# Kernel tuning notes

Hardware: AMD Instinct MI355X
Metric: run time of the kernel (lower is better)

The kernel has to match this reference:

```python
import jax, jax.numpy as jnp
import numpy as np

D_MODEL = 1024
NUM_HEADS = 16
HEAD_DIM = 64
INNER = NUM_HEADS * HEAD_DIM


def setup_inputs() -> dict:
    key = jax.random.key(0)
    k_x, k_q, k_k, k_v, k_o = jax.random.split(key, 5)
    B, T = 4, 2048
    s = 1.0 / np.sqrt(D_MODEL)
    return {
        "x": jax.random.normal(k_x, (B, T, D_MODEL), dtype=jnp.float32),
        "W_q": jax.random.uniform(k_q, (D_MODEL, INNER), dtype=jnp.float32, minval=-s, maxval=s),
        "W_k": jax.random.uniform(k_k, (D_MODEL, INNER), dtype=jnp.float32, minval=-s, maxval=s),
        "W_v": jax.random.uniform(k_v, (D_MODEL, INNER), dtype=jnp.float32, minval=-s, maxval=s),
        "W_o": jax.random.uniform(k_o, (INNER, D_MODEL), dtype=jnp.float32, minval=-s, maxval=s),
    }


def reference(x, W_q, W_k, W_v, W_o):
    B, T, _ = x.shape
    scale = HEAD_DIM ** -0.5
    # project and split heads: [B, H, T, Dh]
    q = (x @ W_q).reshape(B, T, NUM_HEADS, HEAD_DIM).transpose(0, 2, 1, 3)
    k = (x @ W_k).reshape(B, T, NUM_HEADS, HEAD_DIM).transpose(0, 2, 1, 3)
    v = (x @ W_v).reshape(B, T, NUM_HEADS, HEAD_DIM).transpose(0, 2, 1, 3)
    scores = jnp.einsum("bhqd,bhkd->bhqk", q, k) * scale  # [B,H,T,T]
    causal = jnp.tril(jnp.ones((T, T), dtype=bool))
    scores = jnp.where(causal, scores, -jnp.inf)
    probs = jax.nn.softmax(scores, axis=-1)
    ctx = jnp.einsum("bhqk,bhkd->bhqd", probs, v)
    ctx = ctx.transpose(0, 2, 1, 3).reshape(B, T, INNER)
    return ctx @ W_o
```

## Files before the change

kernel.cpp:

```cpp
#include <hip/hip_runtime.h>


typedef short  short8  __attribute__((ext_vector_type(8)));
typedef short  short4v __attribute__((ext_vector_type(4)));
typedef float  floatx4 __attribute__((ext_vector_type(4)));
typedef unsigned uint2v __attribute__((ext_vector_type(2)));

#define T_SZ 2048
#define DM   1024

#define QSCALE 0.18033688011112042f

__device__ __forceinline__ short f2bf(float f) {
  unsigned u = __float_as_uint(f);
  u += 0x7fffu + ((u >> 16) & 1u);
  return (short)(u >> 16);
}

#if defined(__has_builtin) && __has_builtin(__builtin_amdgcn_cvt_pk_bf16_f32)
typedef __bf16 bf16x2_t __attribute__((ext_vector_type(2)));
__device__ __forceinline__ unsigned pack_bf(float lo, float hi) {
  return __builtin_bit_cast(unsigned, __builtin_amdgcn_cvt_pk_bf16_f32(lo, hi));
}
#else
__device__ __forceinline__ unsigned pack_bf(float lo, float hi) {
  return __builtin_amdgcn_perm(__float_as_uint(hi) + 0x8000u,
                               __float_as_uint(lo) + 0x8000u, 0x07060302u);
}
#endif

#if defined(__has_builtin) && __has_builtin(__builtin_amdgcn_exp2f)
__device__ __forceinline__ float fexp2(float x) { return __builtin_amdgcn_exp2f(x); }
#else
__device__ __forceinline__ float fexp2(float x) { return exp2f(x); }
#endif

__device__ __forceinline__ void gll16(const void* g, void* l) {
  __builtin_amdgcn_global_load_lds((const __attribute__((address_space(1))) void*)g,
                                   (__attribute__((address_space(3))) void*)l, 16, 0, 0);
}

__global__ void cvt_kernel(const float* __restrict__ s0, const float* __restrict__ s1,
                           const float* __restrict__ s2, const float* __restrict__ s3,
                           short* __restrict__ dst,
                           const float* __restrict__ x, short* __restrict__ xb) {
  const int tx = threadIdx.x, ty = threadIdx.y;
  if (blockIdx.z == 4) {
    const int tid = ty * 32 + tx;
    const int blk = blockIdx.y * 32 + blockIdx.x;
    int i = (blk * 256 + tid) * 4;
#pragma unroll
    for (int j = 0; j < 8; ++j) {
      const float4 v = *(const float4*)(x + i);
      short4v o;
      o.x = f2bf(v.x); o.y = f2bf(v.y); o.z = f2bf(v.z); o.w = f2bf(v.w);
      *(short4v*)(xb + i) = o;
      i += 1048576;
    }
    return;
  }
  const float* srcs[4] = {s0, s1, s2, s3};
  const float* src = srcs[blockIdx.z];
  short* d = dst + (size_t)blockIdx.z * 1048576;
  __shared__ float tile[32][33];
  const int n_base = blockIdx.x * 32, k_base = blockIdx.y * 32;
#pragma unroll
  for (int j = 0; j < 4; ++j)
    tile[ty + j * 8][tx] = src[(size_t)(k_base + ty + j * 8) * 1024 + n_base + tx];
  __syncthreads();
#pragma unroll
  for (int j = 0; j < 4; ++j)
    d[(size_t)(n_base + ty + j * 8) * 1024 + k_base + tx] = f2bf(tile[tx][ty + j * 8]);
}

template <int MODE>
__global__ void gemm_bt(const short* __restrict__ A, const short* __restrict__ Bt,
                        short* __restrict__ obf, short* __restrict__ vt,
                        float* __restrict__ of, int K) {
  __shared__ short As[128 * 32];
  __shared__ short Bs[128 * 32];
  const int tid  = threadIdx.x;
  const int w    = tid >> 6, lane = tid & 63;
  const int quad = lane >> 4, l15 = lane & 15;
  const int wr   = w >> 1, wc = w & 1;
  const int lid  = (int)blockIdx.y * 64 + (int)blockIdx.x;
  const int m0   = (((lid & 7) + 8 * ((lid >> 3) & 7))) * 128;
  const int n0   = (lid >> 6) * 128;
  const int arow = tid >> 2, apart = tid & 3;

  floatx4 acc[4][4] = {};

  for (int kk = 0; kk < K; kk += 32) {
    gll16(A  + (size_t)(m0 + arow) * K      + kk + apart * 8, &As[tid * 8]);
    gll16(A  + (size_t)(m0 + 64 + arow) * K + kk + apart * 8, &As[(256 + tid) * 8]);
    gll16(Bt + (size_t)(n0 + arow) * K      + kk + apart * 8, &Bs[tid * 8]);
    gll16(Bt + (size_t)(n0 + 64 + arow) * K + kk + apart * 8, &Bs[(256 + tid) * 8]);
    __syncthreads();
    short8 af[4], bfr[4];
#pragma unroll
    for (int i = 0; i < 4; ++i)
      af[i] = *(const short8*)&As[(wr * 64 + i * 16 + l15) * 32 + quad * 8];
#pragma unroll
    for (int j = 0; j < 4; ++j)
      bfr[j] = *(const short8*)&Bs[(wc * 64 + j * 16 + l15) * 32 + quad * 8];
#pragma unroll
    for (int i = 0; i < 4; ++i)
#pragma unroll
      for (int j = 0; j < 4; ++j)
        acc[i][j] = __builtin_amdgcn_mfma_f32_16x16x32_bf16(af[i], bfr[j], acc[i][j], 0, 0, 0);
    __syncthreads();
  }

  if (MODE == 0) {
    const int wsel = n0 >> 10;
    const int ncol0 = (n0 & 1023) + wc * 64;
    if (wsel < 2) {
      const float scale = (wsel == 0) ? QSCALE : 1.0f;
      short* outw = obf + (size_t)wsel * (64u * 2048u * 64u);
#pragma unroll
      for (int i = 0; i < 4; ++i) {
        const int row0 = m0 + wr * 64 + i * 16 + quad * 4;
#pragma unroll
        for (int j = 0; j < 4; ++j) {
          const int col = ncol0 + j * 16 + l15;
          const int h = col >> 6, d = col & 63;
#pragma unroll
          for (int r = 0; r < 4; ++r) {
            const int rg = row0 + r;
            const int b = rg >> 11, t = rg & 2047;
            outw[(((size_t)(b * 16 + h) * 2048 + t) << 6) + d] = f2bf(acc[i][j][r] * scale);
          }
        }
      }
    } else {
#pragma unroll
      for (int i = 0; i < 4; ++i) {
        const int row0 = m0 + wr * 64 + i * 16 + quad * 4;
        const int b = row0 >> 11, t = row0 & 2047;
#pragma unroll
        for (int j = 0; j < 4; ++j) {
          const int col = ncol0 + j * 16 + l15;
          const int h = col >> 6, d = col & 63;
          short4v pv;
#pragma unroll
          for (int r = 0; r < 4; ++r) pv[r] = f2bf(acc[i][j][r]);
          *(short4v*)(vt + (((size_t)(b * 16 + h) * 64 + d) << 11) + t) = pv;
        }
      }
    }
  } else {
#pragma unroll
    for (int i = 0; i < 4; ++i) {
      const int row0 = m0 + wr * 64 + i * 16 + quad * 4;
#pragma unroll
      for (int j = 0; j < 4; ++j) {
        const int col = n0 + wc * 64 + j * 16 + l15;
#pragma unroll
        for (int r = 0; r < 4; ++r)
          of[(size_t)(row0 + r) * 1024 + col] = acc[i][j][r];
      }
    }
  }
}

__global__ __launch_bounds__(512, 4) void attn_kernel(
    const short* __restrict__ Qg, const short* __restrict__ Kg,
    const short* __restrict__ Vt, short* __restrict__ ctx) {
  __shared__ short Ks[128 * 72];
  __shared__ short Vs[80 * 136];
  __shared__ short Ps[8 * 32 * 40];

  const int tid  = threadIdx.x;
  const int w    = tid >> 6, lane = tid & 63;
  const int quad = lane >> 4, l15 = lane & 15;
  const int bh = (int)blockIdx.x + 8 * ((int)blockIdx.y & 7);
  const int g  = (int)blockIdx.y >> 3;
  const int qb = (g < 4) ? (7 - g) : (g - 4);
  const int b  = bh >> 4, h = bh & 15;

  const size_t base = (size_t)bh * (T_SZ * 64);
  const short* Qb  = Qg + base;
  const short* Kb  = Kg + base;
  const short* Vtb = Vt + base;
  short* Pw = &Ps[w * 1280];

  const int skr = tid >> 2, skp = (tid & 3) * 16;
  const int svr = tid >> 3, svp = (tid & 7) * 16;

  if (tid < 256) {
    const int rr = 64 + (tid >> 4), cb = (tid & 15) * 8;
    const short vv = (tid < 16) ? (short)0x3F80 : (short)0;
    short8 fill;
#pragma unroll
    for (int j = 0; j < 8; ++j) fill[j] = vv;
    *(short8*)&Vs[rr * 136 + cb] = fill;
  }

  const int rowA = qb * 256 + w * 32;
  const int rowB = rowA + 16;
  const int ktmax = 2 * qb + 2;

  const short8 qA0 = *(const short8*)(Qb + (size_t)(rowA + l15) * 64 + quad * 8);
  const short8 qA1 = *(const short8*)(Qb + (size_t)(rowA + l15) * 64 + 32 + quad * 8);
  const short8 qB0 = *(const short8*)(Qb + (size_t)(rowB + l15) * 64 + quad * 8);
  const short8 qB1 = *(const short8*)(Qb + (size_t)(rowB + l15) * 64 + 32 + quad * 8);

  floatx4 OA[4] = {}, OB[4] = {};
  floatx4 O5A = {}, O5B = {};

  short8 kR[2], vR[2];
  kR[0] = *(const short8*)(Kb + (size_t)skr * 64 + skp);
  kR[1] = *(const short8*)(Kb + (size_t)skr * 64 + skp + 8);
  vR[0] = *(const short8*)(Vtb + (size_t)svr * 2048 + svp);
  vR[1] = *(const short8*)(Vtb + (size_t)svr * 2048 + svp + 8);

  for (int kt = 0; kt < ktmax; ++kt) {
    const int k0 = kt << 7;
    __syncthreads();
    *(short8*)&Ks[skr * 72 + skp]     = kR[0];
    *(short8*)&Ks[skr * 72 + skp + 8] = kR[1];
    *(short8*)&Vs[svr * 136 + svp]     = vR[0];
    *(short8*)&Vs[svr * 136 + svp + 8] = vR[1];
    if (kt + 1 < ktmax) {
      const int kn = (kt + 1) << 7;
      kR[0] = *(const short8*)(Kb + (size_t)(kn + skr) * 64 + skp);
      kR[1] = *(const short8*)(Kb + (size_t)(kn + skr) * 64 + skp + 8);
      vR[0] = *(const short8*)(Vtb + (size_t)svr * 2048 + kn + svp);
      vR[1] = *(const short8*)(Vtb + (size_t)svr * 2048 + kn + svp + 8);
    }
    __syncthreads();

    const int dkA = rowA - k0;
    if (dkA < 0) continue;
    const int dkB = dkA + 16;
    const int limA = dkA + l15, limB = limA + 16;
    const int naA = min(8, (dkA >> 4) + 1), nchA = (naA + 1) >> 1;
    const int naB = min(8, (dkB >> 4) + 1), nchB = (naB + 1) >> 1;

#pragma unroll
    for (int c = 0; c < 4; ++c) {
      if (c < nchB) {
#pragma unroll
        for (int mm = 0; mm < 2; ++mm) {
          const int mt = 2 * c + mm;
          const int pa = l15 * 40 + mm * 16 + quad * 4;
          const int pb = (16 + l15) * 40 + mm * 16 + quad * 4;
          const bool aB = (mt * 16 < dkB + 16);
          const bool aA = (mt * 16 < dkA + 16);
          if (aB) {
            const short8 kf0 = *(const short8*)&Ks[(mt * 16 + l15) * 72 + quad * 8];
            const short8 kf1 = *(const short8*)&Ks[(mt * 16 + l15) * 72 + 32 + quad * 8];
            {
              floatx4 s = {};
              s = __builtin_amdgcn_mfma_f32_16x16x32_bf16(kf0, qB0, s, 0, 0, 0);
              s = __builtin_amdgcn_mfma_f32_16x16x32_bf16(kf1, qB1, s, 0, 0, 0);
              if (mt * 16 + 15 > dkB) {
#pragma unroll
                for (int r = 0; r < 4; ++r)
                  if (mt * 16 + quad * 4 + r > limB) s[r] = -1e30f;
              }
              floatx4 e;
#pragma unroll
              for (int r = 0; r < 4; ++r) e[r] = fexp2(s[r]);
              uint2v pd;
              pd.x = pack_bf(e[0], e[1]);
              pd.y = pack_bf(e[2], e[3]);
              *(uint2v*)&Pw[pb] = pd;
            }
            if (c < nchA) {
              if (aA) {
                floatx4 s = {};
                s = __builtin_amdgcn_mfma_f32_16x16x32_bf16(kf0, qA0, s, 0, 0, 0);
                s = __builtin_amdgcn_mfma_f32_16x16x32_bf16(kf1, qA1, s, 0, 0, 0);
                if (mt * 16 + 15 > dkA) {
#pragma unroll
                  for (int r = 0; r < 4; ++r)
                    if (mt * 16 + quad * 4 + r > limA) s[r] = -1e30f;
                }
                floatx4 e;
#pragma unroll
                for (int r = 0; r < 4; ++r) e[r] = fexp2(s[r]);
                uint2v pd;
                pd.x = pack_bf(e[0], e[1]);
                pd.y = pack_bf(e[2], e[3]);
                *(uint2v*)&Pw[pa] = pd;
              } else {
                uint2v z; z.x = 0; z.y = 0;
                *(uint2v*)&Pw[pa] = z;
              }
            }
          } else {
            uint2v z; z.x = 0; z.y = 0;
            *(uint2v*)&Pw[pb] = z;
            if (c < nchA) *(uint2v*)&Pw[pa] = z;
          }
        }
        const int vcol = c * 32 + quad * 8;
        const short8 vfl = *(const short8*)&Vs[(64 + l15) * 136 + vcol];
        short8 vf[4];
#pragma unroll
        for (int dt = 0; dt < 4; ++dt)
          vf[dt] = *(const short8*)&Vs[(dt * 16 + l15) * 136 + vcol];
        const short8 pfB = *(const short8*)&Pw[(16 + l15) * 40 + quad * 8];
#pragma unroll
        for (int dt = 0; dt < 4; ++dt)
          OB[dt] = __builtin_amdgcn_mfma_f32_16x16x32_bf16(vf[dt], pfB, OB[dt], 0, 0, 0);
        O5B = __builtin_amdgcn_mfma_f32_16x16x32_bf16(vfl, pfB, O5B, 0, 0, 0);
        if (c < nchA) {
          const short8 pfA = *(const short8*)&Pw[l15 * 40 + quad * 8];
#pragma unroll
          for (int dt = 0; dt < 4; ++dt)
            OA[dt] = __builtin_amdgcn_mfma_f32_16x16x32_bf16(vf[dt], pfA, OA[dt], 0, 0, 0);
          O5A = __builtin_amdgcn_mfma_f32_16x16x32_bf16(vfl, pfA, O5A, 0, 0, 0);
        }
      }
    }
  }

  {
    const float lA = __shfl(O5A[0], l15);
    const float invA = 1.0f / lA;
    const int t = rowA + l15;
    short* cb = ctx + (((size_t)(b * T_SZ + t)) << 10) + h * 64 + quad * 4;
#pragma unroll
    for (int dt = 0; dt < 4; ++dt) {
      short4v o4;
#pragma unroll
      for (int r = 0; r < 4; ++r) o4[r] = f2bf(OA[dt][r] * invA);
      *(short4v*)(cb + dt * 16) = o4;
    }
  }
  {
    const float lB = __shfl(O5B[0], l15);
    const float invB = 1.0f / lB;
    const int t = rowB + l15;
    short* cb = ctx + (((size_t)(b * T_SZ + t)) << 10) + h * 64 + quad * 4;
#pragma unroll
    for (int dt = 0; dt < 4; ++dt) {
      short4v o4;
#pragma unroll
      for (int r = 0; r < 4; ++r) o4[r] = f2bf(OB[dt][r] * invB);
      *(short4v*)(cb + dt * 16) = o4;
    }
  }
}

extern "C" void kernel_launch(void* const* d_in, const int* in_sizes, int n_in,
                              void* d_out, int out_size, void* d_ws, size_t ws_size,
                              hipStream_t stream) {
  const float* x  = (const float*)d_in[0];
  const float* Wq = (const float*)d_in[1];
  const float* Wk = (const float*)d_in[2];
  const float* Wv = (const float*)d_in[3];
  const float* Wo = (const float*)d_in[4];
  float* out = (float*)d_out;

  short* ws  = (short*)d_ws;
  short* xb  = ws;
  short* Wt  = ws + 8388608;
  short* Qb  = Wt + 4 * 1048576;
  short* Kb  = Qb + 8388608;
  short* Vt  = Kb + 8388608;
  short* ctx = xb;

  cvt_kernel<<<dim3(32, 32, 5), dim3(32, 8), 0, stream>>>(Wq, Wk, Wv, Wo, Wt, x, xb);
  gemm_bt<0><<<dim3(64, 24), 256, 0, stream>>>(xb, Wt, Qb, Vt, nullptr, 1024);
  attn_kernel<<<dim3(8, 64), 512, 0, stream>>>(Qb, Kb, Vt, ctx);
  gemm_bt<1><<<dim3(64, 8), 256, 0, stream>>>(ctx, Wt + 3 * 1048576, nullptr, nullptr, out, 1024);
}
```

Baseline: 242.8 us.

## Replace QKV projection GEMM with transposed 128x256 double-buffered pipelined kernel

Adds a new QKV projection kernel that computes the transposed product (weights as rows, tokens as columns). It uses 512-thread blocks with 128x256 tiles and a 64-wide K step, XOR-swizzled LDS, and double-buffered direct global-to-LDS loads. Explicit barriers, waitcnts and setprio interleave MFMA work with the next stage's loads. An XCD-aware block mapping is meant to improve L2 locality. The transposed orientation lets V be written as Vt along tokens, at the cost of strided scalar stores for V and strided short4 stores for Q/K.

```diff
diff --git a/kernel.cpp b/kernel.cpp
--- a/kernel.cpp
+++ b/kernel.cpp
@@ -39,6 +39,11 @@
   __builtin_amdgcn_global_load_lds((const __attribute__((address_space(1))) void*)g,
                                    (__attribute__((address_space(3))) void*)l, 16, 0, 0);
 }
+
+#define SBAR() asm volatile("s_barrier" ::: "memory")
+#define WLG()  asm volatile("s_waitcnt lgkmcnt(0)" ::: "memory")
+#define WV6()  asm volatile("s_waitcnt vmcnt(6)" ::: "memory")
+#define WV0()  asm volatile("s_waitcnt vmcnt(0)" ::: "memory")
 
 __global__ void cvt_kernel(const float* __restrict__ s0, const float* __restrict__ s1,
                            const float* __restrict__ s2, const float* __restrict__ s3,
@@ -71,6 +76,131 @@
 #pragma unroll
   for (int j = 0; j < 4; ++j)
     d[(size_t)(n_base + ty + j * 8) * 1024 + k_base + tx] = f2bf(tile[tx][ty + j * 8]);
+}
+
+__global__ __launch_bounds__(512, 2) void gemm_qkvT(
+    const short* __restrict__ Wt, const short* __restrict__ xb,
+    short* __restrict__ obf, short* __restrict__ vt) {
+  __shared__ short As[2 * 128 * 64];
+  __shared__ short Bs[2 * 256 * 64];
+  const int tid  = threadIdx.x;
+  const int w    = tid >> 6, lane = tid & 63;
+  const int quad = lane >> 4, l15 = lane & 15;
+  const int wr   = w >> 2, wc = w & 3;
+  const int fx   = l15 & 7;
+  const int lid  = (int)blockIdx.x;
+  const int xcd  = lid & 7, idx = lid >> 3;
+  const int m0   = (idx >> 2) * 128;
+  const int n0   = (xcd * 4 + (idx & 3)) * 256;
+  const int srow = tid >> 3;
+  const int scol = ((tid & 7) ^ (srow & 7)) * 8;
+
+  const short* Ag = Wt + (size_t)(m0 + srow) * 1024 + scol;
+  const short* Bg = xb + (size_t)(n0 + srow) * 1024 + scol;
+
+  floatx4 acc[4][4] = {};
+  short8 af[2][2], bf[4][2];
+
+#define STG_A(slot, kb) do { \
+    short* _lb = &As[(slot) * 8192 + tid * 8]; \
+    gll16(Ag + (kb), _lb); \
+    gll16(Ag + (size_t)(64 * 1024) + (kb), _lb + 4096); \
+  } while (0)
+#define STG_B(slot, h, kb) do { \
+    short* _lb = &Bs[(slot) * 16384 + (h) * 8192 + tid * 8]; \
+    const short* _gp = Bg + (size_t)(h) * (128 * 1024) + (kb); \
+    gll16(_gp, _lb); \
+    gll16(_gp + (size_t)(64 * 1024), _lb + 4096); \
+  } while (0)
+#define LDA2(slot, ih) do { \
+    _Pragma("unroll") for (int ii = 0; ii < 2; ++ii) \
+    _Pragma("unroll") for (int s = 0; s < 2; ++s) \
+      af[ii][s] = *(const short8*)&As[(slot) * 8192 + \
+          (wr * 64 + (ih) * 32 + ii * 16 + l15) * 64 + ((s * 4 + quad) ^ fx) * 8]; \
+  } while (0)
+#define LDB8(slot) do { \
+    _Pragma("unroll") for (int j = 0; j < 4; ++j) \
+    _Pragma("unroll") for (int s = 0; s < 2; ++s) \
+      bf[j][s] = *(const short8*)&Bs[(slot) * 16384 + \
+          (wc * 64 + j * 16 + l15) * 64 + ((s * 4 + quad) ^ fx) * 8]; \
+  } while (0)
+#define MMQ(ih, jh) do { \
+    __builtin_amdgcn_s_setprio(1); \
+    _Pragma("unroll") for (int ii = 0; ii < 2; ++ii) \
+    _Pragma("unroll") for (int jj = 0; jj < 2; ++jj) \
+    _Pragma("unroll") for (int s = 0; s < 2; ++s) \
+      acc[(ih) * 2 + ii][(jh) * 2 + jj] = __builtin_amdgcn_mfma_f32_16x16x32_bf16( \
+          af[ii][s], bf[(jh) * 2 + jj][s], acc[(ih) * 2 + ii][(jh) * 2 + jj], 0, 0, 0); \
+    __builtin_amdgcn_s_setprio(0); \
+  } while (0)
+
+  STG_B(0, 0, 0);  STG_B(0, 1, 0);  STG_A(0, 0);
+  STG_B(1, 0, 64); STG_B(1, 1, 64); STG_A(1, 64);
+  WV6(); SBAR();
+
+  for (int t = 0; t < 8; ++t) {
+    const int kn2 = (2 * t + 2) * 64;
+    const int kn3 = (2 * t + 3) * 64;
+    const bool mre = (t < 7);
+    LDA2(0, 0); LDB8(0);
+    SBAR(); WLG(); MMQ(0, 0); SBAR();
+    if (mre) STG_B(0, 0, kn2);
+    SBAR(); MMQ(0, 1); SBAR();
+    LDA2(0, 1);
+    if (mre) STG_B(0, 1, kn2);
+    SBAR(); WLG(); MMQ(1, 0); SBAR();
+    if (mre) { STG_A(0, kn2); WV6(); } else { WV0(); }
+    SBAR(); MMQ(1, 1); SBAR();
+    LDA2(1, 0); LDB8(1);
+    SBAR(); WLG(); MMQ(0, 0); SBAR();
+    if (mre) STG_B(1, 0, kn3);
+    SBAR(); MMQ(0, 1); SBAR();
+    LDA2(1, 1);
+    if (mre) STG_B(1, 1, kn3);
+    SBAR(); WLG(); MMQ(1, 0); SBAR();
+    if (mre) { STG_A(1, kn3); WV6(); }
+    SBAR(); MMQ(1, 1); SBAR();
+  }
+
+  const int wsel = m0 >> 10;
+  const int nn0  = (m0 & 1023) + wr * 64;
+  if (wsel < 2) {
+    const float scale = (wsel == 0) ? QSCALE : 1.0f;
+    short* outw = obf + (size_t)wsel * (64u * 2048u * 64u);
+#pragma unroll
+    for (int i = 0; i < 4; ++i) {
+      const int nn = nn0 + i * 16 + quad * 4;
+      const int h = nn >> 6, d = nn & 63;
+#pragma unroll
+      for (int j = 0; j < 4; ++j) {
+        const int tg = n0 + wc * 64 + j * 16 + l15;
+        const int b = tg >> 11, tt = tg & 2047;
+        short4v o4;
+#pragma unroll
+        for (int r = 0; r < 4; ++r) o4[r] = f2bf(acc[i][j][r] * scale);
+        *(short4v*)(outw + (((size_t)(b * 16 + h) * 2048 + tt) << 6) + d) = o4;
+      }
+    }
+  } else {
+#pragma unroll
+    for (int i = 0; i < 4; ++i) {
+      const int nn = nn0 + i * 16 + quad * 4;
+      const int h = nn >> 6, d = nn & 63;
+#pragma unroll
+      for (int j = 0; j < 4; ++j) {
+        const int tg = n0 + wc * 64 + j * 16 + l15;
+        const int b = tg >> 11, tt = tg & 2047;
+#pragma unroll
+        for (int r = 0; r < 4; ++r)
+          vt[(((size_t)(b * 16 + h) * 64 + d + r) << 11) + tt] = f2bf(acc[i][j][r]);
+      }
+    }
+  }
+#undef STG_A
+#undef STG_B
+#undef LDA2
+#undef LDB8
+#undef MMQ
 }
 
 template <int MODE>
@@ -364,7 +494,7 @@
   short* ctx = xb;
 
   cvt_kernel<<<dim3(32, 32, 5), dim3(32, 8), 0, stream>>>(Wq, Wk, Wv, Wo, Wt, x, xb);
-  gemm_bt<0><<<dim3(64, 24), 256, 0, stream>>>(xb, Wt, Qb, Vt, nullptr, 1024);
+  gemm_qkvT<<<dim3(768), 512, 0, stream>>>(Wt, xb, Qb, Vt);
   attn_kernel<<<dim3(8, 64), 512, 0, stream>>>(Qb, Kb, Vt, ctx);
   gemm_bt<1><<<dim3(64, 8), 256, 0, stream>>>(ctx, Wt + 3 * 1048576, nullptr, nullptr, out, 1024);
 }
```

New measurement: 241.1 us. About the same (-0.7%).

## Replace GEMM with double-buffered 128x256 tile kernel using swizzled LDS and XCD mapping

Applied to the files above, without the earlier changes.

The simple 128x128 tile GEMM, which synchronises on every 32-wide K step, is replaced by an 8-wave kernel. It uses 128x256 tiles with BK=64, double-buffers LDS fills through global_load_lds, and issues explicit vmcnt waits and barriers so loads overlap the MFMA phases. It also XOR-swizzles the LDS layout to avoid bank conflicts, maps blocks to XCDs for L2 locality, and swaps operands (weights as A) so the epilogues can write vectorised rows. The aim is to cut the load latency and synchronisation overhead of the projection GEMMs. The cost is more LDS use, hand-tuned waitcnt ordering that is fragile, and V-transpose stores that become scalar.

```diff
diff --git a/kernel.cpp b/kernel.cpp
--- a/kernel.cpp
+++ b/kernel.cpp
@@ -39,6 +39,11 @@
   __builtin_amdgcn_global_load_lds((const __attribute__((address_space(1))) void*)g,
                                    (__attribute__((address_space(3))) void*)l, 16, 0, 0);
 }
+
+#define SBAR() asm volatile("s_barrier" ::: "memory")
+#define WLG()  asm volatile("s_waitcnt lgkmcnt(0)" ::: "memory")
+#define WV6()  asm volatile("s_waitcnt vmcnt(6)" ::: "memory")
+#define WV0()  asm volatile("s_waitcnt vmcnt(0)" ::: "memory")
 
 __global__ void cvt_kernel(const float* __restrict__ s0, const float* __restrict__ s1,
                            const float* __restrict__ s2, const float* __restrict__ s3,
@@ -74,93 +79,148 @@
 }
 
 template <int MODE>
-__global__ void gemm_bt(const short* __restrict__ A, const short* __restrict__ Bt,
-                        short* __restrict__ obf, short* __restrict__ vt,
-                        float* __restrict__ of, int K) {
-  __shared__ short As[128 * 32];
-  __shared__ short Bs[128 * 32];
+__global__ __launch_bounds__(512, 2) void gemm8(
+    const short* __restrict__ A, const short* __restrict__ B,
+    short* __restrict__ obf, short* __restrict__ vt, float* __restrict__ of) {
+  __shared__ short As[2 * 128 * 64];
+  __shared__ short Bs[2 * 256 * 64];
   const int tid  = threadIdx.x;
   const int w    = tid >> 6, lane = tid & 63;
   const int quad = lane >> 4, l15 = lane & 15;
-  const int wr   = w >> 1, wc = w & 1;
-  const int lid  = (int)blockIdx.y * 64 + (int)blockIdx.x;
-  const int m0   = (((lid & 7) + 8 * ((lid >> 3) & 7))) * 128;
-  const int n0   = (lid >> 6) * 128;
-  const int arow = tid >> 2, apart = tid & 3;
+  const int wr   = w >> 2, wc = w & 3;
+  const int fx   = l15 & 7;
+  const int lid  = (int)blockIdx.x;
+  const int xcd  = lid & 7, idx = lid >> 3;
+  const int m0   = (idx >> 2) * 128;
+  const int n0   = (xcd * 4 + (idx & 3)) * 256;
+  const int srow = tid >> 3;
+  const int scol = ((tid & 7) ^ (srow & 7)) * 8;
+
+  const short* Ag = A + (size_t)(m0 + srow) * 1024 + scol;
+  const short* Bg = B + (size_t)(n0 + srow) * 1024 + scol;
 
   floatx4 acc[4][4] = {};
-
-  for (int kk = 0; kk < K; kk += 32) {
-    gll16(A  + (size_t)(m0 + arow) * K      + kk + apart * 8, &As[tid * 8]);
-    gll16(A  + (size_t)(m0 + 64 + arow) * K + kk + apart * 8, &As[(256 + tid) * 8]);
-    gll16(Bt + (size_t)(n0 + arow) * K      + kk + apart * 8, &Bs[tid * 8]);
-    gll16(Bt + (size_t)(n0 + 64 + arow) * K + kk + apart * 8, &Bs[(256 + tid) * 8]);
-    __syncthreads();
-    short8 af[4], bfr[4];
-#pragma unroll
-    for (int i = 0; i < 4; ++i)
-      af[i] = *(const short8*)&As[(wr * 64 + i * 16 + l15) * 32 + quad * 8];
-#pragma unroll
-    for (int j = 0; j < 4; ++j)
-      bfr[j] = *(const short8*)&Bs[(wc * 64 + j * 16 + l15) * 32 + quad * 8];
-#pragma unroll
-    for (int i = 0; i < 4; ++i)
-#pragma unroll
-      for (int j = 0; j < 4; ++j)
-        acc[i][j] = __builtin_amdgcn_mfma_f32_16x16x32_bf16(af[i], bfr[j], acc[i][j], 0, 0, 0);
-    __syncthreads();
-  }
-
-  if (MODE == 0) {
-    const int wsel = n0 >> 10;
-    const int ncol0 = (n0 & 1023) + wc * 64;
+  short8 af[4][2], bf[4][2];
+
+#define STG_A(slot, kb) do { \
+    short* _lb = &As[(slot) * 8192 + tid * 8]; \
+    const short* _gp = Ag + (kb); \
+    gll16(_gp, _lb); \
+    gll16(_gp + (size_t)(64 * 1024), _lb + 4096); \
+  } while (0)
+#define STG_B(slot, kb) do { \
+    short* _lb = &Bs[(slot) * 16384 + tid * 8]; \
+    const short* _gp = Bg + (kb); \
+    gll16(_gp,                         _lb); \
+    gll16(_gp + (size_t)( 64 * 1024), _lb + 4096); \
+    gll16(_gp + (size_t)(128 * 1024), _lb + 8192); \
+    gll16(_gp + (size_t)(192 * 1024), _lb + 12288); \
+  } while (0)
+#define LDA_ALL(slot) do { \
+    _Pragma("unroll") for (int ii = 0; ii < 4; ++ii) \
+    _Pragma("unroll") for (int s = 0; s < 2; ++s) \
+      af[ii][s] = *(const short8*)&As[(slot) * 8192 + \
+          (wr * 64 + ii * 16 + l15) * 64 + ((s * 4 + quad) ^ fx) * 8]; \
+  } while (0)
+#define LDB_ALL(slot) do { \
+    _Pragma("unroll") for (int j = 0; j < 4; ++j) \
+    _Pragma("unroll") for (int s = 0; s < 2; ++s) \
+      bf[j][s] = *(const short8*)&Bs[(slot) * 16384 + \
+          (wc * 64 + j * 16 + l15) * 64 + ((s * 4 + quad) ^ fx) * 8]; \
+  } while (0)
+#define MMH(ih) do { \
+    __builtin_amdgcn_s_setprio(1); \
+    _Pragma("unroll") for (int i2 = 0; i2 < 2; ++i2) \
+    _Pragma("unroll") for (int j = 0; j < 4; ++j) \
+    _Pragma("unroll") for (int s = 0; s < 2; ++s) \
+      acc[(ih) * 2 + i2][j] = __builtin_amdgcn_mfma_f32_16x16x32_bf16( \
+          af[(ih) * 2 + i2][s], bf[j][s], acc[(ih) * 2 + i2][j], 0, 0, 0); \
+    __builtin_amdgcn_s_setprio(0); \
+  } while (0)
+
+  STG_B(0, 0);  STG_A(0, 0);
+  STG_B(1, 64); STG_A(1, 64);
+  WV6(); SBAR();
+
+  for (int t = 0; t < 8; ++t) {
+    const int kn2 = (2 * t + 2) * 64;
+    const int kn3 = (2 * t + 3) * 64;
+    const bool mre = (t < 7);
+    LDA_ALL(0); LDB_ALL(0);
+    SBAR(); WLG();
+    MMH(0);
+    SBAR();
+    if (mre) STG_B(0, kn2);
+    if (mre) STG_A(0, kn2);
+    MMH(1);
+    if (mre) WV6(); else WV0();
+    SBAR();
+    LDA_ALL(1); LDB_ALL(1);
+    SBAR(); WLG();
+    MMH(0);
+    SBAR();
+    if (mre) STG_B(1, kn3);
+    if (mre) STG_A(1, kn3);
+    MMH(1);
+    if (mre) WV6();
+    SBAR();
+  }
+
+  if constexpr (MODE == 0) {
+    const int wsel = m0 >> 10;
+    const int nn0  = (m0 & 1023) + wr * 64;
     if (wsel < 2) {
       const float scale = (wsel == 0) ? QSCALE : 1.0f;
       short* outw = obf + (size_t)wsel * (64u * 2048u * 64u);
 #pragma unroll
       for (int i = 0; i < 4; ++i) {
-        const int row0 = m0 + wr * 64 + i * 16 + quad * 4;
+        const int nn = nn0 + i * 16 + quad * 4;
+        const int h = nn >> 6, d = nn & 63;
 #pragma unroll
         for (int j = 0; j < 4; ++j) {
-          const int col = ncol0 + j * 16 + l15;
-          const int h = col >> 6, d = col & 63;
-#pragma unroll
-          for (int r = 0; r < 4; ++r) {
-            const int rg = row0 + r;
-            const int b = rg >> 11, t = rg & 2047;
-            outw[(((size_t)(b * 16 + h) * 2048 + t) << 6) + d] = f2bf(acc[i][j][r] * scale);
-          }
+          const int tg = n0 + wc * 64 + j * 16 + l15;
+          const int b = tg >> 11, tt = tg & 2047;
+          short4v o4;
+#pragma unroll
+          for (int r = 0; r < 4; ++r) o4[r] = f2bf(acc[i][j][r] * scale);
+          *(short4v*)(outw + (((size_t)(b * 16 + h) * 2048 + tt) << 6) + d) = o4;
         }
       }
     } else {
 #pragma unroll
       for (int i = 0; i < 4; ++i) {
-        const int row0 = m0 + wr * 64 + i * 16 + quad * 4;
-        const int b = row0 >> 11, t = row0 & 2047;
+        const int nn = nn0 + i * 16 + quad * 4;
+        const int h = nn >> 6, d = nn & 63;
 #pragma unroll
         for (int j = 0; j < 4; ++j) {
-          const int col = ncol0 + j * 16 + l15;
-          const int h = col >> 6, d = col & 63;
-          short4v pv;
-#pragma unroll
-          for (int r = 0; r < 4; ++r) pv[r] = f2bf(acc[i][j][r]);
-          *(short4v*)(vt + (((size_t)(b * 16 + h) * 64 + d) << 11) + t) = pv;
+          const int tg = n0 + wc * 64 + j * 16 + l15;
+          const int b = tg >> 11, tt = tg & 2047;
+#pragma unroll
+          for (int r = 0; r < 4; ++r)
+            vt[(((size_t)(b * 16 + h) * 64 + d + r) << 11) + tt] = f2bf(acc[i][j][r]);
         }
       }
     }
   } else {
+    const int nn0 = m0 + wr * 64;
 #pragma unroll
     for (int i = 0; i < 4; ++i) {
-      const int row0 = m0 + wr * 64 + i * 16 + quad * 4;
+      const int nn = nn0 + i * 16 + quad * 4;
 #pragma unroll
       for (int j = 0; j < 4; ++j) {
-        const int col = n0 + wc * 64 + j * 16 + l15;
-#pragma unroll
-        for (int r = 0; r < 4; ++r)
-          of[(size_t)(row0 + r) * 1024 + col] = acc[i][j][r];
+        const int tg = n0 + wc * 64 + j * 16 + l15;
+        float4 o4;
+        o4.x = acc[i][j][0]; o4.y = acc[i][j][1];
+        o4.z = acc[i][j][2]; o4.w = acc[i][j][3];
+        *(float4*)(of + (size_t)tg * 1024 + nn) = o4;
       }
     }
   }
+#undef STG_A
+#undef STG_B
+#undef LDA_ALL
+#undef LDB_ALL
+#undef MMH
 }
 
 __global__ __launch_bounds__(512, 4) void attn_kernel(
@@ -364,7 +424,7 @@
   short* ctx = xb;
 
   cvt_kernel<<<dim3(32, 32, 5), dim3(32, 8), 0, stream>>>(Wq, Wk, Wv, Wo, Wt, x, xb);
-  gemm_bt<0><<<dim3(64, 24), 256, 0, stream>>>(xb, Wt, Qb, Vt, nullptr, 1024);
+  gemm8<0><<<dim3(768), 512, 0, stream>>>(Wt, xb, Qb, Vt, nullptr);
   attn_kernel<<<dim3(8, 64), 512, 0, stream>>>(Qb, Kb, Vt, ctx);
-  gemm_bt<1><<<dim3(64, 8), 256, 0, stream>>>(ctx, Wt + 3 * 1048576, nullptr, nullptr, out, 1024);
-}
+  gemm8<1><<<dim3(256), 512, 0, stream>>>(Wt + 3 * 1048576, ctx, nullptr, nullptr, out);
+}
```

Result: faster. 236.7 us (-2.5%).
